# Performance work log

Hardware: AMD Instinct MI355X
Metric: run time of the kernel (lower is better)

The kernel has to match this reference:

```python
import jax, jax.numpy as jnp
import numpy as np

N = 50000          # nodes
DEG = 8            # per-node in/out degree
E = N * DEG        # fwd edges (rev = reversed fwd)
H = 128            # hidden_dim
T = 4              # towers
F = H // T         # per-tower F_in (divide_input=True)
FO = H // T        # per-tower F_out
L = 2              # num_layers
IN_DIM = 128
OUT_DIM = 32
AVG_LOG = float(np.log(DEG + 1.0))  # avg of log(deg+1) from deg histogram (all deg==8)
BN_EPS = 1e-5
STD_EPS = 1e-5


def setup_inputs() -> dict:
    key = jax.random.key(0)
    ks = jax.random.split(key, 10)
    x = jax.random.normal(ks[0], (N, IN_DIM), jnp.float32)
    # every node appears exactly DEG times as dst and as src -> deg histogram delta at 8
    dst = jnp.repeat(jnp.arange(N, dtype=jnp.int32), DEG)
    src = jax.random.permutation(ks[1], dst)
    edge_fwd = jnp.stack([src, dst])  # [2, E]

    def rn(k, shape):
        return jax.random.normal(k, shape, jnp.float32) * 0.05

    return dict(
        x=x,
        W_in=rn(ks[2], (IN_DIM, H)), b_in=jnp.zeros((H,), jnp.float32),
        # [layer, relation(fwd/rev), tower, ...]
        pre_W=rn(ks[3], (L, 2, T, 2 * F, F)), pre_b=jnp.zeros((L, 2, T, F), jnp.float32),
        post_W=rn(ks[4], (L, 2, T, 13 * F, FO)), post_b=jnp.zeros((L, 2, T, FO), jnp.float32),
        lin_W=rn(ks[5], (L, 2, H, H)), lin_b=jnp.zeros((L, 2, H), jnp.float32),
        bn_gamma=jnp.ones((L, H), jnp.float32), bn_beta=jnp.zeros((L, H), jnp.float32),
        mlp_W1=rn(ks[6], (H, H)), mlp_b1=jnp.zeros((H,), jnp.float32),
        mlp_W2=rn(ks[7], (H, OUT_DIM)), mlp_b2=jnp.zeros((OUT_DIM,), jnp.float32),
        edge_fwd=edge_fwd,
    )


def _pna(x, src, dst, pre_W, pre_b, post_W, post_b, lin_W, lin_b):
    """One PNAConv (divide_input=True, pre/post_layers=1, no edge attr)."""
    xt = x.reshape(N, T, F)                                   # [N,T,F]
    # message: cat([x_i (dst), x_j (src)]) -> per-tower pre-MLP
    h = jnp.concatenate([xt[dst], xt[src]], axis=-1)          # [E,T,2F]
    m = jnp.einsum('etf,tfg->etg', h, pre_W) + pre_b          # [E,T,F]
    # multi-aggregator scatter reduce over destination nodes
    deg = jax.ops.segment_sum(jnp.ones((m.shape[0],), x.dtype), dst, N)
    degc = jnp.maximum(deg, 1.0)
    inv = (1.0 / degc)[:, None, None]
    mean = jax.ops.segment_sum(m, dst, N) * inv
    mean2 = jax.ops.segment_sum(m * m, dst, N) * inv
    std = jnp.sqrt(jax.nn.relu(mean2 - mean * mean) + STD_EPS)
    mn = jax.ops.segment_min(m, dst, N)
    mx = jax.ops.segment_max(m, dst, N)
    agg = jnp.concatenate([mean, mn, mx, std], axis=-1)       # [N,T,4F]
    # degree scalers: amplification, attenuation, identity
    ld = jnp.log(degc + 1.0)[:, None, None]
    agg = jnp.concatenate([agg * (ld / AVG_LOG), agg * (AVG_LOG / ld), agg], axis=-1)  # [N,T,12F]
    out = jnp.concatenate([xt, agg], axis=-1)                 # [N,T,13F]
    out = jnp.einsum('ntf,tfg->ntg', out, post_W) + post_b    # [N,T,FO]
    out = out.reshape(N, T * FO)
    return out @ lin_W + lin_b                                # [N,H]


def _bn(x, g, b):
    mu = x.mean(0)
    var = x.var(0)  # biased, as torch BatchNorm normalization
    return g * (x - mu) * jax.lax.rsqrt(var + BN_EPS) + b


def reference(x, W_in, b_in, pre_W, pre_b, post_W, post_b, lin_W, lin_b,
              bn_gamma, bn_beta, mlp_W1, mlp_b1, mlp_W2, mlp_b2, edge_fwd):
    src, dst = edge_fwd[0], edge_fwd[1]
    h = jax.nn.relu(x @ W_in + b_in)
    for l in range(L):
        # HeteroConv sum of fwd relation and rev relation (reversed edges)
        y = (_pna(h, src, dst, pre_W[l, 0], pre_b[l, 0], post_W[l, 0], post_b[l, 0], lin_W[l, 0], lin_b[l, 0])
             + _pna(h, dst, src, pre_W[l, 1], pre_b[l, 1], post_W[l, 1], post_b[l, 1], lin_W[l, 1], lin_b[l, 1]))
        h = jax.nn.relu(_bn(y, bn_gamma[l], bn_beta[l]))
        # dropout omitted (deterministic reference / eval mode)
    return jax.nn.relu(h @ mlp_W1 + mlp_b1) @ mlp_W2 + mlp_b2
```

## Files before the change

kernel.cpp:

```cpp
#include <hip/hip_runtime.h>
#include <hip/hip_fp16.h>
#include <cstddef>
#include <cstdint>

#define NN 50000
#define DEG 8
#define EE (NN*DEG)
#define RT_CNT 3125
#define AG_CNT 1563
#define KSTEPS 36
#define W8L 18432
#define MPAD 132
#define BUILD_BLKS 1563
#define PREP_BLKS (16 + BUILD_BLKS + 50)

typedef __attribute__((ext_vector_type(8))) short short8;
typedef __attribute__((ext_vector_type(4))) float f32x4;

union Pack8 { __half h[8]; __half2 h2[4]; uint4 u; short8 s8; };

__global__ __launch_bounds__(256) void k_prep(
    const float* __restrict__ post_W, const float* __restrict__ pre_W,
    const float* __restrict__ pre_b, const float* __restrict__ post_b,
    const float* __restrict__ lin_W, const float* __restrict__ lin_b,
    __half* __restrict__ Wcp, float* __restrict__ Qw, float* __restrict__ bc,
    const int* __restrict__ ef, int* __restrict__ cnt,
    int* __restrict__ fwd_nbr, int* __restrict__ rev_nbr,
    const float* __restrict__ W_in, __half* __restrict__ Winp,
    const float* __restrict__ mlp_W1, __half* __restrict__ W1p,
    const float* __restrict__ mlp_W2, __half* __restrict__ W2p,
    __half* __restrict__ WbBD) {
    __shared__ float Pf[160 * 33];
    __shared__ float Wl[32 * 128];
    __shared__ float Wt[32 * 32];
    __shared__ float Ps[32 * 32];
    __shared__ float Q[32 * 32];
    __shared__ float T3s[32];
    int tid = threadIdx.x;
    int b = blockIdx.x;
    if (b >= 16 && b < 16 + BUILD_BLKS) {
        int e = (b - 16) * 256 + tid;
        if (e < EE) {
            int s = ef[e], d = ef[EE + e];
            int p = atomicAdd(&cnt[d], 1);
            fwd_nbr[d * DEG + p] = s;
            int q = atomicAdd(&cnt[NN + s], 1);
            rev_nbr[s * DEG + q] = d;
        }
        return;
    }
    if (b >= 16 + BUILD_BLKS) {
        int pid = (b - 16 - BUILD_BLKS) * 256 + tid;
        if (pid < 4608) {
            const float* W; __half* dst; int id; int N;
            if (pid < 2048)      { W = W_in;   dst = Winp; id = pid;        N = 128; }
            else if (pid < 4096) { W = mlp_W1; dst = W1p;  id = pid - 2048; N = 128; }
            else                 { W = mlp_W2; dst = W2p;  id = pid - 4096; N = 32;  }
            int lane = id & 63;
            int ks = (id >> 6) & 3;
            int t = (id >> 6) >> 2;
            int quad = lane >> 4, nl = lane & 15;
            int n = t * 16 + nl;
            Pack8 pk;
#pragma unroll
            for (int e = 0; e < 8; e++)
                pk.h[e] = __float2half(W[(size_t)(ks * 32 + quad * 8 + e) * N + n]);
            *(uint4*)&dst[(size_t)id * 8] = pk.u;
        } else if (pid < 12800) {
            int id = pid - 4608;
            int lane = id & 63, ks = (id >> 6) & 3, t8 = (id >> 8) & 7;
            int rel = (id >> 11) & 1, l = id >> 12;
            int quad = lane >> 4, nl = lane & 15;
            int n = t8 * 16 + nl;
            int tn = n >> 5;
            Pack8 pk;
#pragma unroll
            for (int e = 0; e < 8; e++) {
                int k = ks * 32 + quad * 8 + e;
                float v = 0.f;
                if ((k >> 5) == tn)
                    v = pre_W[(size_t)((((l * 2 + rel) * 4 + tn) * 64) + 32 + (k & 31)) * 32 + (n & 31)];
                pk.h[e] = __float2half(v);
            }
            *(uint4*)&WbBD[((size_t)(l * 2 + rel) * 2048 + (t8 * 4 + ks) * 64 + lane) * 8] = pk.u;
        }
        return;
    }
    int m4 = b;
    int l = m4 >> 3, r = (m4 >> 2) & 1, tw = m4 & 3;
    const float* PW = post_W + (size_t)m4 * 416 * 32;
    for (int i = tid; i < 160 * 32; i += 256) {
        int row = i >> 5, g = i & 31;
        float v;
        if (row < 32) v = PW[row * 32 + g];
        else {
            int rr = row - 32;
            v = PW[(32 + rr) * 32 + g] + PW[(160 + rr) * 32 + g] + PW[(288 + rr) * 32 + g];
        }
        Pf[row * 33 + g] = v;
    }
    for (int i = tid; i < 1024; i += 256) Wt[i] = pre_W[(size_t)m4 * 2048 + i];
    for (int i = tid; i < 4096; i += 256)
        Wl[i] = lin_W[(size_t)(l * 2 + r) * 16384 + tw * 32 * 128 + i];
    __syncthreads();
    for (int i = tid; i < 1024; i += 256) {
        int g = i >> 5, j = i & 31;
        Ps[i] = Pf[(32 + g) * 33 + j] + Pf[(64 + g) * 33 + j] + Pf[(96 + g) * 33 + j];
    }
    __syncthreads();
    for (int i = tid; i < 1024; i += 256) {
        int f = i >> 5, j = i & 31;
        float acc = Pf[f * 33 + j];
#pragma unroll
        for (int g = 0; g < 32; g++) acc += Wt[f * 32 + g] * Ps[g * 32 + j];
        Q[i] = acc;
    }
    if (tid < 32) {
        int j = tid;
        float v = post_b[m4 * 32 + j];
#pragma unroll
        for (int g = 0; g < 32; g++) v += pre_b[m4 * 32 + g] * Ps[g * 32 + j];
        T3s[j] = v;
    }
    __syncthreads();
    for (int u = tid; u < 2048; u += 256) {
        int lane = u & 63, t = (u >> 6) & 7, s = u >> 9;
        int quad = lane >> 4, nl = lane & 15;
        int n = t * 16 + nl;
        Pack8 pk;
#pragma unroll
        for (int e = 0; e < 8; e++) {
            int f = quad * 8 + e;
            const float* Pr = &Pf[((s + 1) * 32 + f) * 33];
            float acc = 0.f;
#pragma unroll
            for (int j = 0; j < 32; j++) acc += Pr[j] * Wl[j * 128 + n];
            pk.h[e] = __float2half(acc);
        }
        int ks = 4 + r * 16 + tw * 4 + s;
        *(uint4*)&Wcp[((size_t)l * W8L + (t * KSTEPS + ks) * 64 + lane) * 8] = pk.u;
    }
    for (int i = tid; i < 4096; i += 256) {
        int f = i >> 7, n = i & 127;
        float acc = 0.f;
#pragma unroll
        for (int j = 0; j < 32; j++) acc += Q[f * 32 + j] * Wl[j * 128 + n];
        atomicAdd(&Qw[(size_t)l * 16384 + (tw * 32 + f) * 128 + n], acc);
    }
    if (tid < 128) {
        float v = 0.f;
#pragma unroll
        for (int j = 0; j < 32; j++) v += T3s[j] * Wl[j * 128 + tid];
        atomicAdd(&bc[l * 128 + tid], v);
        if ((m4 & 7) == 0)
            atomicAdd(&bc[l * 128 + tid],
                      lin_b[(2 * l) * 128 + tid] + lin_b[(2 * l + 1) * 128 + tid]);
    }
}

__global__ __launch_bounds__(256) void k_in_fused(
    const float* __restrict__ X, const __half* __restrict__ Wp,
    const float* __restrict__ b, const __half* __restrict__ WbBDp,
    __half* __restrict__ H, __half* __restrict__ Bplanes,
    const float* __restrict__ Qw, __half* __restrict__ Wcp, int gWave) {
    __shared__ __half Sh[4][16 * MPAD];
    int tid = threadIdx.x, wv = tid >> 6, lane = tid & 63;
    if (blockIdx.x >= gWave) {
        int gid = (blockIdx.x - gWave) * 256 + tid;
        if (gid < 4096) {
            int pl = gid & 63, t = (gid >> 6) & 7, ks = (gid >> 9) & 3, l = gid >> 11;
            int quad = pl >> 4;
            int n = t * 16 + (pl & 15);
            Pack8 pk;
#pragma unroll
            for (int e = 0; e < 8; e++)
                pk.h[e] = __float2half(Qw[(size_t)l * 16384 + (ks * 32 + quad * 8 + e) * 128 + n]);
            *(uint4*)&Wcp[((size_t)l * W8L + (t * KSTEPS + ks) * 64 + pl) * 8] = pk.u;
        }
        return;
    }
    int rt = blockIdx.x * 4 + wv;
    if (rt >= RT_CNT) rt = RT_CNT - 1;
    int mm = lane & 15, quad = lane >> 4;
    short8 a[4];
#pragma unroll
    for (int ks = 0; ks < 4; ks++) {
        const float4* p = (const float4*)&X[(size_t)(rt * 16 + mm) * 128 + ks * 32 + quad * 8];
        float4 v0 = p[0], v1 = p[1];
        Pack8 pk;
        pk.h[0] = __float2half(v0.x); pk.h[1] = __float2half(v0.y);
        pk.h[2] = __float2half(v0.z); pk.h[3] = __float2half(v0.w);
        pk.h[4] = __float2half(v1.x); pk.h[5] = __float2half(v1.y);
        pk.h[6] = __float2half(v1.z); pk.h[7] = __float2half(v1.w);
        a[ks] = pk.s8;
    }
    const short8* Bb = (const short8*)Wp + lane;
    f32x4 acc[8];
#pragma unroll
    for (int t = 0; t < 8; t++) acc[t] = (f32x4){0.f, 0.f, 0.f, 0.f};
#pragma unroll
    for (int ks = 0; ks < 4; ks++)
#pragma unroll
        for (int t = 0; t < 8; t++)
            acc[t] = __builtin_amdgcn_mfma_f32_16x16x32_f16(
                a[ks], Bb[(t * 4 + ks) * 64], acc[t], 0, 0, 0);
    __half* T = Sh[wv];
#pragma unroll
    for (int t = 0; t < 8; t++) {
        int n = t * 16 + mm;
        float bias = b[n];
#pragma unroll
        for (int r = 0; r < 4; r++)
            T[(quad * 4 + r) * MPAD + n] = __float2half(fmaxf(acc[t][r] + bias, 0.f));
    }
#pragma unroll
    for (int it = 0; it < 4; it++) {
        int idx = it * 64 + lane;
        int row = idx >> 4, col = (idx & 15) * 8;
        *(uint4*)&H[(size_t)(rt * 16 + row) * 128 + col] = *(uint4*)&T[row * MPAD + col];
    }
    short8 a2[4];
#pragma unroll
    for (int ks = 0; ks < 4; ks++)
        a2[ks] = *(const short8*)&T[mm * MPAD + ks * 32 + quad * 8];
#pragma unroll
    for (int rel = 0; rel < 2; rel++) {
        const short8* Bd = (const short8*)WbBDp + (size_t)rel * 2048 + lane;
        f32x4 ac[8];
#pragma unroll
        for (int t = 0; t < 8; t++) ac[t] = (f32x4){0.f, 0.f, 0.f, 0.f};
#pragma unroll
        for (int ks = 0; ks < 4; ks++)
#pragma unroll
            for (int t = 0; t < 8; t++)
                ac[t] = __builtin_amdgcn_mfma_f32_16x16x32_f16(
                    a2[ks], Bd[(t * 4 + ks) * 64], ac[t], 0, 0, 0);
#pragma unroll
        for (int t = 0; t < 8; t++) {
            int n = t * 16 + mm;
#pragma unroll
            for (int r = 0; r < 4; r++)
                T[(quad * 4 + r) * MPAD + n] = __float2half(ac[t][r]);
        }
        __half* Bp = Bplanes + (size_t)rel * NN * 128;
#pragma unroll
        for (int it = 0; it < 4; it++) {
            int idx = it * 64 + lane;
            int row = idx >> 4, col = (idx & 15) * 8;
            *(uint4*)&Bp[(size_t)(rt * 16 + row) * 128 + col] = *(uint4*)&T[row * MPAD + col];
        }
    }
}

template<int V>
__global__ __launch_bounds__(256) void k_preB_mfma(
    const __half* __restrict__ Hin, const float* __restrict__ Yf,
    const float* __restrict__ bns, const float* __restrict__ bns2,
    const float* __restrict__ gamma, const float* __restrict__ beta,
    __half* __restrict__ Hout, const __half* __restrict__ WbBDp,
    __half* __restrict__ Bplanes) {
    __shared__ __half Sh[4][16 * MPAD];
    __shared__ float sc[128], sh[128];
    int tid = threadIdx.x, wv = tid >> 6, lane = tid & 63;
    int rt = blockIdx.x * 4 + wv;
    if (rt >= RT_CNT) rt = RT_CNT - 1;
    if (V == 2) {
        if (tid < 128) {
            float mu = bns[tid] * (1.f / NN);
            float var = bns2[tid] * (1.f / NN) - mu * mu;
            float s = gamma[tid] * rsqrtf(var + 1e-5f);
            sc[tid] = s;
            sh[tid] = beta[tid] - mu * s;
        }
        __syncthreads();
    }
    int mm = lane & 15, quad = lane >> 4;
    short8 a[4];
#pragma unroll
    for (int ks = 0; ks < 4; ks++) {
        int c0 = ks * 32 + quad * 8;
        size_t base = (size_t)(rt * 16 + mm) * 128 + c0;
        if (V == 1) {
            Pack8 pk; pk.u = *(const uint4*)&Hin[base];
            a[ks] = pk.s8;
        } else {
            const float4* p = (const float4*)&Yf[base];
            float4 v0 = p[0], v1 = p[1];
            float4 s0 = *(const float4*)&sc[c0], s1 = *(const float4*)&sc[c0 + 4];
            float4 f0 = *(const float4*)&sh[c0], f1 = *(const float4*)&sh[c0 + 4];
            Pack8 pk;
            pk.h[0] = __float2half(fmaxf(s0.x * v0.x + f0.x, 0.f));
            pk.h[1] = __float2half(fmaxf(s0.y * v0.y + f0.y, 0.f));
            pk.h[2] = __float2half(fmaxf(s0.z * v0.z + f0.z, 0.f));
            pk.h[3] = __float2half(fmaxf(s0.w * v0.w + f0.w, 0.f));
            pk.h[4] = __float2half(fmaxf(s1.x * v1.x + f1.x, 0.f));
            pk.h[5] = __float2half(fmaxf(s1.y * v1.y + f1.y, 0.f));
            pk.h[6] = __float2half(fmaxf(s1.z * v1.z + f1.z, 0.f));
            pk.h[7] = __float2half(fmaxf(s1.w * v1.w + f1.w, 0.f));
            *(uint4*)&Hout[base] = pk.u;
            a[ks] = pk.s8;
        }
    }
    __half* T = Sh[wv];
#pragma unroll
    for (int rel = 0; rel < 2; rel++) {
        const short8* Bb = (const short8*)WbBDp + (size_t)rel * 2048 + lane;
        f32x4 acc[8];
#pragma unroll
        for (int t = 0; t < 8; t++) acc[t] = (f32x4){0.f, 0.f, 0.f, 0.f};
#pragma unroll
        for (int ks = 0; ks < 4; ks++)
#pragma unroll
            for (int t = 0; t < 8; t++)
                acc[t] = __builtin_amdgcn_mfma_f32_16x16x32_f16(
                    a[ks], Bb[(t * 4 + ks) * 64], acc[t], 0, 0, 0);
#pragma unroll
        for (int t = 0; t < 8; t++) {
            int n = t * 16 + mm;
#pragma unroll
            for (int r = 0; r < 4; r++)
                T[(quad * 4 + r) * MPAD + n] = __float2half(acc[t][r]);
        }
        __half* Bp = Bplanes + (size_t)rel * NN * 128;
#pragma unroll
        for (int it = 0; it < 4; it++) {
            int idx = it * 64 + lane;
            int row = idx >> 4, col = (idx & 15) * 8;
            *(uint4*)&Bp[(size_t)(rt * 16 + row) * 128 + col] = *(uint4*)&T[row * MPAD + col];
        }
    }
}

__global__ __launch_bounds__(512) void k_agg_gemm(
    const __half* __restrict__ hbuf, const __half* __restrict__ Bplanes,
    const int* __restrict__ fwd_nbr, const int* __restrict__ rev_nbr,
    const __half* __restrict__ Wcp, const float* __restrict__ bc,
    float* __restrict__ Y, float* __restrict__ bnsum, float* __restrict__ bnsum2) {
    __shared__ __half Spack[32 * 128 * 8];
    int tid = threadIdx.x;
    int blk = blockIdx.x;
    int lane = tid & 63, wv = tid >> 6;
    int G = tid >> 4;
    int f16 = tid & 15;
    int tw = f16 >> 2, quad = f16 & 3;
    int fo = f16 * 8;
    int pos = quad * 32 + (G ^ quad ^ ((tw & 1) << 2));
    int mB = lane & 15, qB = lane >> 4;
    int t = wv;
    int nodeg = blk * 32 + G;
    if (nodeg >= NN) nodeg = NN - 1;

    Pack8 axt[2][4];
#pragma unroll
    for (int mt = 0; mt < 2; mt++) {
        int nd = blk * 32 + mt * 16 + mB;
        if (nd >= NN) nd = NN - 1;
#pragma unroll
        for (int ks = 0; ks < 4; ks++)
            axt[mt][ks].u = *(const uint4*)&hbuf[(size_t)nd * 128 + ks * 32 + qB * 8];
    }
    {
        const int4* nf = (const int4*)&fwd_nbr[nodeg * 8];
        const int4* nr = (const int4*)&rev_nbr[nodeg * 8];
        int4 a0 = nf[0], a1 = nf[1], b0v = nr[0], b1v = nr[1];
        int idx0[8] = {a0.x, a0.y, a0.z, a0.w, a1.x, a1.y, a1.z, a1.w};
        int idx1[8] = {b0v.x, b0v.y, b0v.z, b0v.w, b1v.x, b1v.y, b1v.z, b1v.w};
        Pack8 r0[8], r1[8];
        const __half* Bp1 = Bplanes + (size_t)NN * 128;
#pragma unroll
        for (int k = 0; k < 8; k++)
            r0[k].u = *(const uint4*)&Bplanes[(size_t)idx0[k] * 128 + fo];
#pragma unroll
        for (int k = 0; k < 8; k++)
            r1[k].u = *(const uint4*)&Bp1[(size_t)idx1[k] * 128 + fo];
#pragma unroll
        for (int rel = 0; rel < 2; rel++) {
            Pack8* rr = rel ? r1 : r0;
            float sS[8], qS[8], mnS[8], mxS[8];
#pragma unroll
            for (int j = 0; j < 8; j++) {
                sS[j] = 0.f; qS[j] = 0.f; mnS[j] = 1e30f; mxS[j] = -1e30f;
            }
#pragma unroll
            for (int k = 0; k < 8; k++) {
#pragma unroll
                for (int j2 = 0; j2 < 4; j2++) {
                    __half2 h = rr[k].h2[j2];
                    float a = __half2float(__low2half(h));
                    float b = __half2float(__high2half(h));
                    int j0 = 2 * j2, j1 = j0 + 1;
                    sS[j0] += a; qS[j0] += a * a;
                    mnS[j0] = fminf(mnS[j0], a); mxS[j0] = fmaxf(mxS[j0], a);
                    sS[j1] += b; qS[j1] += b * b;
                    mnS[j1] = fminf(mnS[j1], b); mxS[j1] = fmaxf(mxS[j1], b);
                }
            }
            Pack8 mean, stdv, mnp, mxp;
#pragma unroll
            for (int j = 0; j < 8; j++) {
                float Bm = sS[j] * 0.125f;
                mean.h[j] = __float2half(Bm);
                stdv.h[j] = __float2half(
                    sqrtf(fmaxf(qS[j] * 0.125f - Bm * Bm, 0.f) + 1e-5f));
                mnp.h[j] = __float2half(mnS[j]);
                mxp.h[j] = __float2half(mxS[j]);
            }
            int ksb = rel * 16 + tw * 4;
            *(uint4*)&Spack[((size_t)(ksb + 0) * 128 + pos) * 8] = mean.u;
            *(uint4*)&Spack[((size_t)(ksb + 1) * 128 + pos) * 8] = mnp.u;
            *(uint4*)&Spack[((size_t)(ksb + 2) * 128 + pos) * 8] = mxp.u;
            *(uint4*)&Spack[((size_t)(ksb + 3) * 128 + pos) * 8] = stdv.u;
        }
    }
    __syncthreads();
    const short8* Bb = (const short8*)Wcp + lane;
    f32x4 acc0 = (f32x4){0.f, 0.f, 0.f, 0.f};
    f32x4 acc1 = (f32x4){0.f, 0.f, 0.f, 0.f};
    short8 p[6];
#pragma unroll
    for (int dd = 0; dd < 6; dd++) p[dd] = Bb[((size_t)t * KSTEPS + dd) * 64];
    __builtin_amdgcn_s_setprio(1);
#pragma unroll
    for (int ks = 0; ks < KSTEPS; ks++) {
        short8 a0f, a1f;
        if (ks < 4) {
            a0f = axt[0][ks].s8;
            a1f = axt[1][ks].s8;
        } else {
            int ss = ks - 4;
            int twk = (ss >> 2) & 3;
            int posr = qB * 32 + (mB ^ qB ^ ((twk & 1) << 2));
            const __half* row = &Spack[((size_t)ss * 128 + posr) * 8];
            a0f = *(const short8*)row;
            a1f = *(const short8*)(row + 16 * 8);
        }
        acc0 = __builtin_amdgcn_mfma_f32_16x16x32_f16(a0f, p[ks % 6], acc0, 0, 0, 0);
        acc1 = __builtin_amdgcn_mfma_f32_16x16x32_f16(a1f, p[ks % 6], acc1, 0, 0, 0);
        if (ks + 6 < KSTEPS) p[ks % 6] = Bb[((size_t)t * KSTEPS + ks + 6) * 64];
    }
    __builtin_amdgcn_s_setprio(0);
#pragma unroll
    for (int mt = 0; mt < 2; mt++) {
        f32x4 acc = mt ? acc1 : acc0;
        int n = t * 16 + mB;
        float bias = bc[n];
        float ls = 0.f, ls2 = 0.f;
#pragma unroll
        for (int r = 0; r < 4; r++) {
            int node = blk * 32 + mt * 16 + qB * 4 + r;
            if (node < NN) {
                float v = acc[r] + bias;
                Y[(size_t)node * 128 + n] = v;
                ls += v; ls2 += v * v;
            }
        }
        ls += __shfl_xor(ls, 16); ls += __shfl_xor(ls, 32);
        ls2 += __shfl_xor(ls2, 16); ls2 += __shfl_xor(ls2, 32);
        if (qB == 0) {
            atomicAdd(&bnsum[n], ls);
            atomicAdd(&bnsum2[n], ls2);
        }
    }
}

__global__ __launch_bounds__(256) void k_mlp_mfma(
    const float* __restrict__ Yb, const float* __restrict__ bns,
    const float* __restrict__ bns2, const float* __restrict__ gamma,
    const float* __restrict__ beta, const __half* __restrict__ W1p,
    const float* __restrict__ b1, const __half* __restrict__ W2p,
    const float* __restrict__ b2, float* __restrict__ out) {
    __shared__ __half Sh[4][16 * MPAD];
    __shared__ float sc[128], sh[128];
    int tid = threadIdx.x, wv = tid >> 6, lane = tid & 63;
    int rt = blockIdx.x * 4 + wv;
    if (rt >= RT_CNT) rt = RT_CNT - 1;
    if (tid < 128) {
        float mu = bns[tid] * (1.f / NN);
        float var = bns2[tid] * (1.f / NN) - mu * mu;
        float s = gamma[tid] * rsqrtf(var + 1e-5f);
        sc[tid] = s;
        sh[tid] = beta[tid] - mu * s;
    }
    __syncthreads();
    int mm = lane & 15, quad = lane >> 4;
    short8 a[4];
#pragma unroll
    for (int ks = 0; ks < 4; ks++) {
        int c0 = ks * 32 + quad * 8;
        const float4* p = (const float4*)&Yb[(size_t)(rt * 16 + mm) * 128 + c0];
        float4 v0 = p[0], v1 = p[1];
        float4 s0 = *(const float4*)&sc[c0], s1 = *(const float4*)&sc[c0 + 4];
        float4 f0 = *(const float4*)&sh[c0], f1 = *(const float4*)&sh[c0 + 4];
        Pack8 pk;
        pk.h[0] = __float2half(fmaxf(s0.x * v0.x + f0.x, 0.f));
        pk.h[1] = __float2half(fmaxf(s0.y * v0.y + f0.y, 0.f));
        pk.h[2] = __float2half(fmaxf(s0.z * v0.z + f0.z, 0.f));
        pk.h[3] = __float2half(fmaxf(s0.w * v0.w + f0.w, 0.f));
        pk.h[4] = __float2half(fmaxf(s1.x * v1.x + f1.x, 0.f));
        pk.h[5] = __float2half(fmaxf(s1.y * v1.y + f1.y, 0.f));
        pk.h[6] = __float2half(fmaxf(s1.z * v1.z + f1.z, 0.f));
        pk.h[7] = __float2half(fmaxf(s1.w * v1.w + f1.w, 0.f));
        a[ks] = pk.s8;
    }
    const short8* B1 = (const short8*)W1p + lane;
    f32x4 acc[8];
#pragma unroll
    for (int t = 0; t < 8; t++) acc[t] = (f32x4){0.f, 0.f, 0.f, 0.f};
#pragma unroll
    for (int ks = 0; ks < 4; ks++)
#pragma unroll
        for (int t = 0; t < 8; t++)
            acc[t] = __builtin_amdgcn_mfma_f32_16x16x32_f16(
                a[ks], B1[(t * 4 + ks) * 64], acc[t], 0, 0, 0);
    __half* T = Sh[wv];
#pragma unroll
    for (int t = 0; t < 8; t++) {
        int n = t * 16 + mm;
        float bias = b1[n];
#pragma unroll
        for (int r = 0; r < 4; r++)
            T[(quad * 4 + r) * MPAD + n] = __float2half(fmaxf(acc[t][r] + bias, 0.f));
    }
    short8 a2[4];
#pragma unroll
    for (int ks = 0; ks < 4; ks++)
        a2[ks] = *(const short8*)&T[mm * MPAD + ks * 32 + quad * 8];
    const short8* B2 = (const short8*)W2p + lane;
    f32x4 acc2[2];
#pragma unroll
    for (int t = 0; t < 2; t++) acc2[t] = (f32x4){0.f, 0.f, 0.f, 0.f};
#pragma unroll
    for (int ks = 0; ks < 4; ks++)
#pragma unroll
        for (int t = 0; t < 2; t++)
            acc2[t] = __builtin_amdgcn_mfma_f32_16x16x32_f16(
                a2[ks], B2[(t * 4 + ks) * 64], acc2[t], 0, 0, 0);
#pragma unroll
    for (int t = 0; t < 2; t++) {
        int n = t * 16 + mm;
        float bias = b2[n];
#pragma unroll
        for (int r = 0; r < 4; r++)
            out[(size_t)(rt * 16 + quad * 4 + r) * 32 + n] = acc2[t][r] + bias;
    }
}

extern "C" void kernel_launch(void* const* d_in, const int* in_sizes, int n_in,
                              void* d_out, int out_size, void* d_ws, size_t ws_size,
                              hipStream_t stream) {
    const float* x      = (const float*)d_in[0];
    const float* W_in   = (const float*)d_in[1];
    const float* b_in   = (const float*)d_in[2];
    const float* pre_W  = (const float*)d_in[3];
    const float* pre_b  = (const float*)d_in[4];
    const float* post_W = (const float*)d_in[5];
    const float* post_b = (const float*)d_in[6];
    const float* lin_W  = (const float*)d_in[7];
    const float* lin_b  = (const float*)d_in[8];
    const float* bn_g   = (const float*)d_in[9];
    const float* bn_b   = (const float*)d_in[10];
    const float* mlp_W1 = (const float*)d_in[11];
    const float* mlp_b1 = (const float*)d_in[12];
    const float* mlp_W2 = (const float*)d_in[13];
    const float* mlp_b2 = (const float*)d_in[14];
    const int*   edge   = (const int*)d_in[15];
    float* out = (float*)d_out;

    char* w = (char*)d_ws;
    const size_t plane = (size_t)NN * 128 * sizeof(float);
    __half* hbuf = (__half*)w; w += plane / 2;
    float* ybuf = (float*)w; w += plane;
    __half* Bpl = (__half*)w; w += plane;
    int* fwd_nbr = (int*)w; w += (size_t)NN * DEG * sizeof(int);
    int* rev_nbr = (int*)w; w += (size_t)NN * DEG * sizeof(int);
    char* zbase = w;
    int* cnt     = (int*)w; w += (size_t)2 * NN * sizeof(int);
    float* Qw    = (float*)w; w += (size_t)2 * 128 * 128 * sizeof(float);
    float* bc    = (float*)w; w += 2 * 128 * sizeof(float);
    float* bns   = (float*)w; w += 4 * 128 * sizeof(float);
    size_t zsize = (size_t)(w - zbase);
    __half* Wcp  = (__half*)w; w += (size_t)2 * KSTEPS * 32 * 128 * sizeof(__half);
    __half* Winp = (__half*)w; w += (size_t)128 * 128 * sizeof(__half);
    __half* W1p  = (__half*)w; w += (size_t)128 * 128 * sizeof(__half);
    __half* W2p  = (__half*)w; w += (size_t)128 * 32 * sizeof(__half);
    __half* WbBD = (__half*)w; w += (size_t)4 * 128 * 128 * sizeof(__half);

    const int gWave = (RT_CNT + 3) / 4;

    (void)hipMemsetAsync(zbase, 0, zsize, stream);
    k_prep<<<PREP_BLKS, 256, 0, stream>>>(
        post_W, pre_W, pre_b, post_b, lin_W, lin_b, Wcp, Qw, bc,
        edge, cnt, fwd_nbr, rev_nbr,
        W_in, Winp, mlp_W1, W1p, mlp_W2, W2p, WbBD);

    k_in_fused<<<gWave + 16, 256, 0, stream>>>(x, Winp, b_in, WbBD, hbuf, Bpl,
                                               Qw, Wcp, gWave);

    k_agg_gemm<<<AG_CNT, 512, 0, stream>>>(
        hbuf, Bpl, fwd_nbr, rev_nbr, Wcp, bc, ybuf, bns, bns + 128);
    k_preB_mfma<2><<<gWave, 256, 0, stream>>>(
        nullptr, ybuf, bns, bns + 128, bn_g, bn_b, hbuf,
        WbBD + (size_t)2 * 128 * 128, Bpl);
    k_agg_gemm<<<AG_CNT, 512, 0, stream>>>(
        hbuf, Bpl, fwd_nbr, rev_nbr, Wcp + (size_t)KSTEPS * 32 * 128,
        bc + 128, ybuf, bns + 256, bns + 384);

    k_mlp_mfma<<<gWave, 256, 0, stream>>>(ybuf, bns + 256, bns + 384,
                                          bn_g + 128, bn_b + 128,
                                          W1p, mlp_b1, W2p, mlp_b2, out);
}
```

Before: 436.5 us.

## Fuse post-prep stages into one cooperative persistent kernel with grid syncs

```diff
diff --git a/kernel.cpp b/kernel.cpp
--- a/kernel.cpp
+++ b/kernel.cpp
@@ -1,7 +1,10 @@
 #include <hip/hip_runtime.h>
 #include <hip/hip_fp16.h>
+#include <hip/hip_cooperative_groups.h>
 #include <cstddef>
 #include <cstdint>
+
+namespace cg = cooperative_groups;
 
 #define NN 50000
 #define DEG 8
@@ -158,29 +161,10 @@
     }
 }
 
-__global__ __launch_bounds__(256) void k_in_fused(
-    const float* __restrict__ X, const __half* __restrict__ Wp,
+__device__ __forceinline__ void in_fused_wave(
+    int rt, int lane, const float* __restrict__ X, const __half* __restrict__ Wp,
     const float* __restrict__ b, const __half* __restrict__ WbBDp,
-    __half* __restrict__ H, __half* __restrict__ Bplanes,
-    const float* __restrict__ Qw, __half* __restrict__ Wcp, int gWave) {
-    __shared__ __half Sh[4][16 * MPAD];
-    int tid = threadIdx.x, wv = tid >> 6, lane = tid & 63;
-    if (blockIdx.x >= gWave) {
-        int gid = (blockIdx.x - gWave) * 256 + tid;
-        if (gid < 4096) {
-            int pl = gid & 63, t = (gid >> 6) & 7, ks = (gid >> 9) & 3, l = gid >> 11;
-            int quad = pl >> 4;
-            int n = t * 16 + (pl & 15);
-            Pack8 pk;
-#pragma unroll
-            for (int e = 0; e < 8; e++)
-                pk.h[e] = __float2half(Qw[(size_t)l * 16384 + (ks * 32 + quad * 8 + e) * 128 + n]);
-            *(uint4*)&Wcp[((size_t)l * W8L + (t * KSTEPS + ks) * 64 + pl) * 8] = pk.u;
-        }
-        return;
-    }
-    int rt = blockIdx.x * 4 + wv;
-    if (rt >= RT_CNT) rt = RT_CNT - 1;
+    __half* __restrict__ H, __half* __restrict__ Bplanes, __half* T) {
     int mm = lane & 15, quad = lane >> 4;
     short8 a[4];
 #pragma unroll
@@ -204,7 +188,6 @@
         for (int t = 0; t < 8; t++)
             acc[t] = __builtin_amdgcn_mfma_f32_16x16x32_f16(
                 a[ks], Bb[(t * 4 + ks) * 64], acc[t], 0, 0, 0);
-    __half* T = Sh[wv];
 #pragma unroll
     for (int t = 0; t < 8; t++) {
         int n = t * 16 + mm;
@@ -252,56 +235,33 @@
     }
 }
 
-template<int V>
-__global__ __launch_bounds__(256) void k_preB_mfma(
-    const __half* __restrict__ Hin, const float* __restrict__ Yf,
-    const float* __restrict__ bns, const float* __restrict__ bns2,
-    const float* __restrict__ gamma, const float* __restrict__ beta,
+__device__ __forceinline__ void preB_wave(
+    int rt, int lane, const float* __restrict__ Yf,
+    const float* __restrict__ sc, const float* __restrict__ sh,
     __half* __restrict__ Hout, const __half* __restrict__ WbBDp,
-    __half* __restrict__ Bplanes) {
-    __shared__ __half Sh[4][16 * MPAD];
-    __shared__ float sc[128], sh[128];
-    int tid = threadIdx.x, wv = tid >> 6, lane = tid & 63;
-    int rt = blockIdx.x * 4 + wv;
-    if (rt >= RT_CNT) rt = RT_CNT - 1;
-    if (V == 2) {
-        if (tid < 128) {
-            float mu = bns[tid] * (1.f / NN);
-            float var = bns2[tid] * (1.f / NN) - mu * mu;
-            float s = gamma[tid] * rsqrtf(var + 1e-5f);
-            sc[tid] = s;
-            sh[tid] = beta[tid] - mu * s;
-        }
-        __syncthreads();
-    }
+    __half* __restrict__ Bplanes, __half* T) {
     int mm = lane & 15, quad = lane >> 4;
     short8 a[4];
 #pragma unroll
     for (int ks = 0; ks < 4; ks++) {
         int c0 = ks * 32 + quad * 8;
         size_t base = (size_t)(rt * 16 + mm) * 128 + c0;
-        if (V == 1) {
-            Pack8 pk; pk.u = *(const uint4*)&Hin[base];
-            a[ks] = pk.s8;
-        } else {
-            const float4* p = (const float4*)&Yf[base];
-            float4 v0 = p[0], v1 = p[1];
-            float4 s0 = *(const float4*)&sc[c0], s1 = *(const float4*)&sc[c0 + 4];
-            float4 f0 = *(const float4*)&sh[c0], f1 = *(const float4*)&sh[c0 + 4];
-            Pack8 pk;
-            pk.h[0] = __float2half(fmaxf(s0.x * v0.x + f0.x, 0.f));
-            pk.h[1] = __float2half(fmaxf(s0.y * v0.y + f0.y, 0.f));
-            pk.h[2] = __float2half(fmaxf(s0.z * v0.z + f0.z, 0.f));
-            pk.h[3] = __float2half(fmaxf(s0.w * v0.w + f0.w, 0.f));
-            pk.h[4] = __float2half(fmaxf(s1.x * v1.x + f1.x, 0.f));
-            pk.h[5] = __float2half(fmaxf(s1.y * v1.y + f1.y, 0.f));
-            pk.h[6] = __float2half(fmaxf(s1.z * v1.z + f1.z, 0.f));
-            pk.h[7] = __float2half(fmaxf(s1.w * v1.w + f1.w, 0.f));
-            *(uint4*)&Hout[base] = pk.u;
-            a[ks] = pk.s8;
-        }
-    }
-    __half* T = Sh[wv];
+        const float4* p = (const float4*)&Yf[base];
+        float4 v0 = p[0], v1 = p[1];
+        float4 s0 = *(const float4*)&sc[c0], s1 = *(const float4*)&sc[c0 + 4];
+        float4 f0 = *(const float4*)&sh[c0], f1 = *(const float4*)&sh[c0 + 4];
+        Pack8 pk;
+        pk.h[0] = __float2half(fmaxf(s0.x * v0.x + f0.x, 0.f));
+        pk.h[1] = __float2half(fmaxf(s0.y * v0.y + f0.y, 0.f));
+        pk.h[2] = __float2half(fmaxf(s0.z * v0.z + f0.z, 0.f));
+        pk.h[3] = __float2half(fmaxf(s0.w * v0.w + f0.w, 0.f));
+        pk.h[4] = __float2half(fmaxf(s1.x * v1.x + f1.x, 0.f));
+        pk.h[5] = __float2half(fmaxf(s1.y * v1.y + f1.y, 0.f));
+        pk.h[6] = __float2half(fmaxf(s1.z * v1.z + f1.z, 0.f));
+        pk.h[7] = __float2half(fmaxf(s1.w * v1.w + f1.w, 0.f));
+        *(uint4*)&Hout[base] = pk.u;
+        a[ks] = pk.s8;
+    }
 #pragma unroll
     for (int rel = 0; rel < 2; rel++) {
         const short8* Bb = (const short8*)WbBDp + (size_t)rel * 2048 + lane;
@@ -331,157 +291,12 @@
     }
 }
 
-__global__ __launch_bounds__(512) void k_agg_gemm(
-    const __half* __restrict__ hbuf, const __half* __restrict__ Bplanes,
-    const int* __restrict__ fwd_nbr, const int* __restrict__ rev_nbr,
-    const __half* __restrict__ Wcp, const float* __restrict__ bc,
-    float* __restrict__ Y, float* __restrict__ bnsum, float* __restrict__ bnsum2) {
-    __shared__ __half Spack[32 * 128 * 8];
-    int tid = threadIdx.x;
-    int blk = blockIdx.x;
-    int lane = tid & 63, wv = tid >> 6;
-    int G = tid >> 4;
-    int f16 = tid & 15;
-    int tw = f16 >> 2, quad = f16 & 3;
-    int fo = f16 * 8;
-    int pos = quad * 32 + (G ^ quad ^ ((tw & 1) << 2));
-    int mB = lane & 15, qB = lane >> 4;
-    int t = wv;
-    int nodeg = blk * 32 + G;
-    if (nodeg >= NN) nodeg = NN - 1;
-
-    Pack8 axt[2][4];
-#pragma unroll
-    for (int mt = 0; mt < 2; mt++) {
-        int nd = blk * 32 + mt * 16 + mB;
-        if (nd >= NN) nd = NN - 1;
-#pragma unroll
-        for (int ks = 0; ks < 4; ks++)
-            axt[mt][ks].u = *(const uint4*)&hbuf[(size_t)nd * 128 + ks * 32 + qB * 8];
-    }
-    {
-        const int4* nf = (const int4*)&fwd_nbr[nodeg * 8];
-        const int4* nr = (const int4*)&rev_nbr[nodeg * 8];
-        int4 a0 = nf[0], a1 = nf[1], b0v = nr[0], b1v = nr[1];
-        int idx0[8] = {a0.x, a0.y, a0.z, a0.w, a1.x, a1.y, a1.z, a1.w};
-        int idx1[8] = {b0v.x, b0v.y, b0v.z, b0v.w, b1v.x, b1v.y, b1v.z, b1v.w};
-        Pack8 r0[8], r1[8];
-        const __half* Bp1 = Bplanes + (size_t)NN * 128;
-#pragma unroll
-        for (int k = 0; k < 8; k++)
-            r0[k].u = *(const uint4*)&Bplanes[(size_t)idx0[k] * 128 + fo];
-#pragma unroll
-        for (int k = 0; k < 8; k++)
-            r1[k].u = *(const uint4*)&Bp1[(size_t)idx1[k] * 128 + fo];
-#pragma unroll
-        for (int rel = 0; rel < 2; rel++) {
-            Pack8* rr = rel ? r1 : r0;
-            float sS[8], qS[8], mnS[8], mxS[8];
-#pragma unroll
-            for (int j = 0; j < 8; j++) {
-                sS[j] = 0.f; qS[j] = 0.f; mnS[j] = 1e30f; mxS[j] = -1e30f;
-            }
-#pragma unroll
-            for (int k = 0; k < 8; k++) {
-#pragma unroll
-                for (int j2 = 0; j2 < 4; j2++) {
-                    __half2 h = rr[k].h2[j2];
-                    float a = __half2float(__low2half(h));
-                    float b = __half2float(__high2half(h));
-                    int j0 = 2 * j2, j1 = j0 + 1;
-                    sS[j0] += a; qS[j0] += a * a;
-                    mnS[j0] = fminf(mnS[j0], a); mxS[j0] = fmaxf(mxS[j0], a);
-                    sS[j1] += b; qS[j1] += b * b;
-                    mnS[j1] = fminf(mnS[j1], b); mxS[j1] = fmaxf(mxS[j1], b);
-                }
-            }
-            Pack8 mean, stdv, mnp, mxp;
-#pragma unroll
-            for (int j = 0; j < 8; j++) {
-                float Bm = sS[j] * 0.125f;
-                mean.h[j] = __float2half(Bm);
-                stdv.h[j] = __float2half(
-                    sqrtf(fmaxf(qS[j] * 0.125f - Bm * Bm, 0.f) + 1e-5f));
-                mnp.h[j] = __float2half(mnS[j]);
-                mxp.h[j] = __float2half(mxS[j]);
-            }
-            int ksb = rel * 16 + tw * 4;
-            *(uint4*)&Spack[((size_t)(ksb + 0) * 128 + pos) * 8] = mean.u;
-            *(uint4*)&Spack[((size_t)(ksb + 1) * 128 + pos) * 8] = mnp.u;
-            *(uint4*)&Spack[((size_t)(ksb + 2) * 128 + pos) * 8] = mxp.u;
-            *(uint4*)&Spack[((size_t)(ksb + 3) * 128 + pos) * 8] = stdv.u;
-        }
-    }
-    __syncthreads();
-    const short8* Bb = (const short8*)Wcp + lane;
-    f32x4 acc0 = (f32x4){0.f, 0.f, 0.f, 0.f};
-    f32x4 acc1 = (f32x4){0.f, 0.f, 0.f, 0.f};
-    short8 p[6];
-#pragma unroll
-    for (int dd = 0; dd < 6; dd++) p[dd] = Bb[((size_t)t * KSTEPS + dd) * 64];
-    __builtin_amdgcn_s_setprio(1);
-#pragma unroll
-    for (int ks = 0; ks < KSTEPS; ks++) {
-        short8 a0f, a1f;
-        if (ks < 4) {
-            a0f = axt[0][ks].s8;
-            a1f = axt[1][ks].s8;
-        } else {
-            int ss = ks - 4;
-            int twk = (ss >> 2) & 3;
-            int posr = qB * 32 + (mB ^ qB ^ ((twk & 1) << 2));
-            const __half* row = &Spack[((size_t)ss * 128 + posr) * 8];
-            a0f = *(const short8*)row;
-            a1f = *(const short8*)(row + 16 * 8);
-        }
-        acc0 = __builtin_amdgcn_mfma_f32_16x16x32_f16(a0f, p[ks % 6], acc0, 0, 0, 0);
-        acc1 = __builtin_amdgcn_mfma_f32_16x16x32_f16(a1f, p[ks % 6], acc1, 0, 0, 0);
-        if (ks + 6 < KSTEPS) p[ks % 6] = Bb[((size_t)t * KSTEPS + ks + 6) * 64];
-    }
-    __builtin_amdgcn_s_setprio(0);
-#pragma unroll
-    for (int mt = 0; mt < 2; mt++) {
-        f32x4 acc = mt ? acc1 : acc0;
-        int n = t * 16 + mB;
-        float bias = bc[n];
-        float ls = 0.f, ls2 = 0.f;
-#pragma unroll
-        for (int r = 0; r < 4; r++) {
-            int node = blk * 32 + mt * 16 + qB * 4 + r;
-            if (node < NN) {
-                float v = acc[r] + bias;
-                Y[(size_t)node * 128 + n] = v;
-                ls += v; ls2 += v * v;
-            }
-        }
-        ls += __shfl_xor(ls, 16); ls += __shfl_xor(ls, 32);
-        ls2 += __shfl_xor(ls2, 16); ls2 += __shfl_xor(ls2, 32);
-        if (qB == 0) {
-            atomicAdd(&bnsum[n], ls);
-            atomicAdd(&bnsum2[n], ls2);
-        }
-    }
-}
-
-__global__ __launch_bounds__(256) void k_mlp_mfma(
-    const float* __restrict__ Yb, const float* __restrict__ bns,
-    const float* __restrict__ bns2, const float* __restrict__ gamma,
-    const float* __restrict__ beta, const __half* __restrict__ W1p,
-    const float* __restrict__ b1, const __half* __restrict__ W2p,
-    const float* __restrict__ b2, float* __restrict__ out) {
-    __shared__ __half Sh[4][16 * MPAD];
-    __shared__ float sc[128], sh[128];
-    int tid = threadIdx.x, wv = tid >> 6, lane = tid & 63;
-    int rt = blockIdx.x * 4 + wv;
-    if (rt >= RT_CNT) rt = RT_CNT - 1;
-    if (tid < 128) {
-        float mu = bns[tid] * (1.f / NN);
-        float var = bns2[tid] * (1.f / NN) - mu * mu;
-        float s = gamma[tid] * rsqrtf(var + 1e-5f);
-        sc[tid] = s;
-        sh[tid] = beta[tid] - mu * s;
-    }
-    __syncthreads();
+__device__ __forceinline__ void mlp_wave(
+    int rt, int lane, const float* __restrict__ Yb,
+    const float* __restrict__ sc, const float* __restrict__ sh,
+    const __half* __restrict__ W1p, const float* __restrict__ b1,
+    const __half* __restrict__ W2p, const float* __restrict__ b2,
+    float* __restrict__ out, __half* T) {
     int mm = lane & 15, quad = lane >> 4;
     short8 a[4];
 #pragma unroll
@@ -512,7 +327,6 @@
         for (int t = 0; t < 8; t++)
             acc[t] = __builtin_amdgcn_mfma_f32_16x16x32_f16(
                 a[ks], B1[(t * 4 + ks) * 64], acc[t], 0, 0, 0);
-    __half* T = Sh[wv];
 #pragma unroll
     for (int t = 0; t < 8; t++) {
         int n = t * 16 + mm;
@@ -543,6 +357,213 @@
         for (int r = 0; r < 4; r++)
             out[(size_t)(rt * 16 + quad * 4 + r) * 32 + n] = acc2[t][r] + bias;
     }
+}
+
+__device__ __forceinline__ void agg_tile(
+    int blk, int tid, const __half* __restrict__ hbuf,
+    const __half* __restrict__ Bplanes,
+    const int* __restrict__ fwd_nbr, const int* __restrict__ rev_nbr,
+    const __half* __restrict__ Wcp, const float* __restrict__ bc,
+    float* __restrict__ Y, float* __restrict__ bnsum, float* __restrict__ bnsum2,
+    __half* __restrict__ Spack) {
+    int lane = tid & 63, wv = tid >> 6;
+    int G = tid >> 4;
+    int f16 = tid & 15;
+    int tw = f16 >> 2, quad = f16 & 3;
+    int fo = f16 * 8;
+    int pos = quad * 32 + (G ^ quad ^ ((tw & 1) << 2));
+    int mB = lane & 15, qB = lane >> 4;
+    int t = wv;
+    int nodeg = blk * 32 + G;
+    if (nodeg >= NN) nodeg = NN - 1;
+
+    Pack8 axt[2][4];
+#pragma unroll
+    for (int mt = 0; mt < 2; mt++) {
+        int nd = blk * 32 + mt * 16 + mB;
+        if (nd >= NN) nd = NN - 1;
+#pragma unroll
+        for (int ks = 0; ks < 4; ks++)
+            axt[mt][ks].u = *(const uint4*)&hbuf[(size_t)nd * 128 + ks * 32 + qB * 8];
+    }
+    {
+        const int4* nf = (const int4*)&fwd_nbr[nodeg * 8];
+        const int4* nr = (const int4*)&rev_nbr[nodeg * 8];
+        int4 a0 = nf[0], a1 = nf[1], b0v = nr[0], b1v = nr[1];
+        int idx0[8] = {a0.x, a0.y, a0.z, a0.w, a1.x, a1.y, a1.z, a1.w};
+        int idx1[8] = {b0v.x, b0v.y, b0v.z, b0v.w, b1v.x, b1v.y, b1v.z, b1v.w};
+        Pack8 r0[8], r1[8];
+        const __half* Bp1 = Bplanes + (size_t)NN * 128;
+#pragma unroll
+        for (int k = 0; k < 8; k++)
+            r0[k].u = *(const uint4*)&Bplanes[(size_t)idx0[k] * 128 + fo];
+#pragma unroll
+        for (int k = 0; k < 8; k++)
+            r1[k].u = *(const uint4*)&Bp1[(size_t)idx1[k] * 128 + fo];
+#pragma unroll
+        for (int rel = 0; rel < 2; rel++) {
+            Pack8* rr = rel ? r1 : r0;
+            float sS[8], qS[8], mnS[8], mxS[8];
+#pragma unroll
+            for (int j = 0; j < 8; j++) {
+                sS[j] = 0.f; qS[j] = 0.f; mnS[j] = 1e30f; mxS[j] = -1e30f;
+            }
+#pragma unroll
+            for (int k = 0; k < 8; k++) {
+#pragma unroll
+                for (int j2 = 0; j2 < 4; j2++) {
+                    __half2 h = rr[k].h2[j2];
+                    float a = __half2float(__low2half(h));
+                    float b = __half2float(__high2half(h));
+                    int j0 = 2 * j2, j1 = j0 + 1;
+                    sS[j0] += a; qS[j0] += a * a;
+                    mnS[j0] = fminf(mnS[j0], a); mxS[j0] = fmaxf(mxS[j0], a);
+                    sS[j1] += b; qS[j1] += b * b;
+                    mnS[j1] = fminf(mnS[j1], b); mxS[j1] = fmaxf(mxS[j1], b);
+                }
+            }
+            Pack8 mean, stdv, mnp, mxp;
+#pragma unroll
+            for (int j = 0; j < 8; j++) {
+                float Bm = sS[j] * 0.125f;
+                mean.h[j] = __float2half(Bm);
+                stdv.h[j] = __float2half(
+                    sqrtf(fmaxf(qS[j] * 0.125f - Bm * Bm, 0.f) + 1e-5f));
+                mnp.h[j] = __float2half(mnS[j]);
+                mxp.h[j] = __float2half(mxS[j]);
+            }
+            int ksb = rel * 16 + tw * 4;
+            *(uint4*)&Spack[((size_t)(ksb + 0) * 128 + pos) * 8] = mean.u;
+            *(uint4*)&Spack[((size_t)(ksb + 1) * 128 + pos) * 8] = mnp.u;
+            *(uint4*)&Spack[((size_t)(ksb + 2) * 128 + pos) * 8] = mxp.u;
+            *(uint4*)&Spack[((size_t)(ksb + 3) * 128 + pos) * 8] = stdv.u;
+        }
+    }
+    __syncthreads();
+    const short8* Bb = (const short8*)Wcp + lane;
+    f32x4 acc0 = (f32x4){0.f, 0.f, 0.f, 0.f};
+    f32x4 acc1 = (f32x4){0.f, 0.f, 0.f, 0.f};
+    short8 p[6];
+#pragma unroll
+    for (int dd = 0; dd < 6; dd++) p[dd] = Bb[((size_t)t * KSTEPS + dd) * 64];
+    __builtin_amdgcn_s_setprio(1);
+#pragma unroll
+    for (int ks = 0; ks < KSTEPS; ks++) {
+        short8 a0f, a1f;
+        if (ks < 4) {
+            a0f = axt[0][ks].s8;
+            a1f = axt[1][ks].s8;
+        } else {
+            int ss = ks - 4;
+            int twk = (ss >> 2) & 3;
+            int posr = qB * 32 + (mB ^ qB ^ ((twk & 1) << 2));
+            const __half* row = &Spack[((size_t)ss * 128 + posr) * 8];
+            a0f = *(const short8*)row;
+            a1f = *(const short8*)(row + 16 * 8);
+        }
+        acc0 = __builtin_amdgcn_mfma_f32_16x16x32_f16(a0f, p[ks % 6], acc0, 0, 0, 0);
+        acc1 = __builtin_amdgcn_mfma_f32_16x16x32_f16(a1f, p[ks % 6], acc1, 0, 0, 0);
+        if (ks + 6 < KSTEPS) p[ks % 6] = Bb[((size_t)t * KSTEPS + ks + 6) * 64];
+    }
+    __builtin_amdgcn_s_setprio(0);
+#pragma unroll
+    for (int mt = 0; mt < 2; mt++) {
+        f32x4 acc = mt ? acc1 : acc0;
+        int n = t * 16 + mB;
+        float bias = bc[n];
+        float ls = 0.f, ls2 = 0.f;
+#pragma unroll
+        for (int r = 0; r < 4; r++) {
+            int node = blk * 32 + mt * 16 + qB * 4 + r;
+            if (node < NN) {
+                float v = acc[r] + bias;
+                Y[(size_t)node * 128 + n] = v;
+                ls += v; ls2 += v * v;
+            }
+        }
+        ls += __shfl_xor(ls, 16); ls += __shfl_xor(ls, 32);
+        ls2 += __shfl_xor(ls2, 16); ls2 += __shfl_xor(ls2, 32);
+        if (qB == 0) {
+            atomicAdd(&bnsum[n], ls);
+            atomicAdd(&bnsum2[n], ls2);
+        }
+    }
+}
+
+__global__ __launch_bounds__(512) void k_mega(
+    const float* __restrict__ X, const __half* __restrict__ Winp,
+    const float* __restrict__ b_in, const __half* __restrict__ WbBD,
+    __half* __restrict__ hbuf, __half* __restrict__ Bpl,
+    const float* __restrict__ Qw, __half* __restrict__ Wcp,
+    const int* __restrict__ fwd_nbr, const int* __restrict__ rev_nbr,
+    const float* __restrict__ bc, float* __restrict__ ybuf,
+    float* __restrict__ bns, const float* __restrict__ bn_g,
+    const float* __restrict__ bn_b,
+    const __half* __restrict__ W1p, const float* __restrict__ b1,
+    const __half* __restrict__ W2p, const float* __restrict__ b2,
+    float* __restrict__ out) {
+    __shared__ __half Spack[32 * 128 * 8];
+    __shared__ float sc[128], sh[128];
+    cg::grid_group grid = cg::this_grid();
+    int tid = threadIdx.x, blk = blockIdx.x, nblk = gridDim.x;
+    int wv = tid >> 6, lane = tid & 63;
+    __half* T = Spack + (size_t)wv * 16 * MPAD;
+
+    for (int rt = blk * 8 + wv; rt < RT_CNT; rt += nblk * 8)
+        in_fused_wave(rt, lane, X, Winp, b_in, WbBD, hbuf, Bpl, T);
+    if (blk >= nblk - 8) {
+        int gid = (blk - (nblk - 8)) * 512 + tid;
+        if (gid < 4096) {
+            int pl = gid & 63, t = (gid >> 6) & 7, ks = (gid >> 9) & 3, l = gid >> 11;
+            int quad = pl >> 4;
+            int n = t * 16 + (pl & 15);
+            Pack8 pk;
+#pragma unroll
+            for (int e = 0; e < 8; e++)
+                pk.h[e] = __float2half(Qw[(size_t)l * 16384 + (ks * 32 + quad * 8 + e) * 128 + n]);
+            *(uint4*)&Wcp[((size_t)l * W8L + (t * KSTEPS + ks) * 64 + pl) * 8] = pk.u;
+        }
+    }
+    grid.sync();
+
+    for (int tile = blk; tile < AG_CNT; tile += nblk) {
+        agg_tile(tile, tid, hbuf, Bpl, fwd_nbr, rev_nbr, Wcp, bc,
+                 ybuf, bns, bns + 128, Spack);
+        __syncthreads();
+    }
+    grid.sync();
+
+    if (tid < 128) {
+        float mu = bns[tid] * (1.f / NN);
+        float var = bns[128 + tid] * (1.f / NN) - mu * mu;
+        float s = bn_g[tid] * rsqrtf(var + 1e-5f);
+        sc[tid] = s;
+        sh[tid] = bn_b[tid] - mu * s;
+    }
+    __syncthreads();
+    for (int rt = blk * 8 + wv; rt < RT_CNT; rt += nblk * 8)
+        preB_wave(rt, lane, ybuf, sc, sh, hbuf,
+                  WbBD + (size_t)2 * 128 * 128, Bpl, T);
+    grid.sync();
+
+    for (int tile = blk; tile < AG_CNT; tile += nblk) {
+        agg_tile(tile, tid, hbuf, Bpl, fwd_nbr, rev_nbr,
+                 Wcp + (size_t)KSTEPS * 32 * 128, bc + 128,
+                 ybuf, bns + 256, bns + 384, Spack);
+        __syncthreads();
+    }
+    grid.sync();
+
+    if (tid < 128) {
+        float mu = bns[256 + tid] * (1.f / NN);
+        float var = bns[384 + tid] * (1.f / NN) - mu * mu;
+        float s = bn_g[128 + tid] * rsqrtf(var + 1e-5f);
+        sc[tid] = s;
+        sh[tid] = bn_b[128 + tid] - mu * s;
+    }
+    __syncthreads();
+    for (int rt = blk * 8 + wv; rt < RT_CNT; rt += nblk * 8)
+        mlp_wave(rt, lane, ybuf, sc, sh, W1p, b1, W2p, b2, out, T);
 }
 
 extern "C" void kernel_launch(void* const* d_in, const int* in_sizes, int n_in,
@@ -585,27 +606,26 @@
     __half* W2p  = (__half*)w; w += (size_t)128 * 32 * sizeof(__half);
     __half* WbBD = (__half*)w; w += (size_t)4 * 128 * 128 * sizeof(__half);
 
-    const int gWave = (RT_CNT + 3) / 4;
-
     (void)hipMemsetAsync(zbase, 0, zsize, stream);
     k_prep<<<PREP_BLKS, 256, 0, stream>>>(
         post_W, pre_W, pre_b, post_b, lin_W, lin_b, Wcp, Qw, bc,
         edge, cnt, fwd_nbr, rev_nbr,
         W_in, Winp, mlp_W1, W1p, mlp_W2, W2p, WbBD);
 
-    k_in_fused<<<gWave + 16, 256, 0, stream>>>(x, Winp, b_in, WbBD, hbuf, Bpl,
-                                               Qw, Wcp, gWave);
-
-    k_agg_gemm<<<AG_CNT, 512, 0, stream>>>(
-        hbuf, Bpl, fwd_nbr, rev_nbr, Wcp, bc, ybuf, bns, bns + 128);
-    k_preB_mfma<2><<<gWave, 256, 0, stream>>>(
-        nullptr, ybuf, bns, bns + 128, bn_g, bn_b, hbuf,
-        WbBD + (size_t)2 * 128 * 128, Bpl);
-    k_agg_gemm<<<AG_CNT, 512, 0, stream>>>(
-        hbuf, Bpl, fwd_nbr, rev_nbr, Wcp + (size_t)KSTEPS * 32 * 128,
-        bc + 128, ybuf, bns + 256, bns + 384);
-
-    k_mlp_mfma<<<gWave, 256, 0, stream>>>(ybuf, bns + 256, bns + 384,
-                                          bn_g + 128, bn_b + 128,
-                                          W1p, mlp_b1, W2p, mlp_b2, out);
+    int maxActive = 0;
+    (void)hipOccupancyMaxActiveBlocksPerMultiprocessor(&maxActive, k_mega, 512, 0);
+    if (maxActive < 1) maxActive = 1;
+    int gridN = maxActive * 256;
+    if (gridN > 512) gridN = 512;
+
+    const float* Qwc = Qw;
+    void* kargs[] = {
+        (void*)&x, (void*)&Winp, (void*)&b_in, (void*)&WbBD,
+        (void*)&hbuf, (void*)&Bpl, (void*)&Qwc, (void*)&Wcp,
+        (void*)&fwd_nbr, (void*)&rev_nbr,
+        (void*)&bc, (void*)&ybuf, (void*)&bns, (void*)&bn_g, (void*)&bn_b,
+        (void*)&W1p, (void*)&mlp_b1, (void*)&W2p, (void*)&mlp_b2, (void*)&out
+    };
+    (void)hipLaunchCooperativeKernel((void*)k_mega, dim3(gridN), dim3(512),
+                                     kargs, 0, stream);
 }
```

After: 675.6 us. 54.8% more time.
